# Performance work log

Hardware: AMD Instinct MI355X
Metric: run time of the kernel (lower is better)

## Reference

```python
import jax, jax.numpy as jnp
import numpy as np

EMB_DIM = 64
TREE_DIM = 128
VOCAB = 10000
SORT_VOCAB = 64
DEPTH = 8  # levels 0..8; leaves are level 0, root is level DEPTH
N_TREES = 256


def _tree_topology(depth):
    # perfect binary tree, nodes laid out leaves-first so the root is the LAST node
    level_sizes = [2 ** (depth - l) for l in range(depth + 1)]
    offsets = np.cumsum([0] + level_sizes)
    n = int(offsets[-1])  # 2^(depth+1)-1
    node_order = np.concatenate([np.full(level_sizes[l], l, np.int64) for l in range(depth + 1)])
    par, chi, eo = [], [], []
    for l in range(1, depth + 1):
        p = offsets[l] + np.arange(level_sizes[l])
        c0 = offsets[l - 1] + 2 * np.arange(level_sizes[l])
        par.append(np.repeat(p, 2))
        chi.append(np.stack([c0, c0 + 1], 1).reshape(-1))
        eo.append(np.full(2 * level_sizes[l], l, np.int64))
    return n, node_order, np.concatenate(par), np.concatenate(chi), np.concatenate(eo)


def setup_inputs():
    key = jax.random.key(0)
    ks = jax.random.split(key, 16)
    n, no, par, chi, eo = _tree_topology(DEPTH)
    offs = np.arange(N_TREES, dtype=np.int64) * n
    node_order = jnp.asarray(np.tile(no, N_TREES))
    parent_idx = jnp.asarray((par[None, :] + offs[:, None]).reshape(-1))
    child_idx = jnp.asarray((chi[None, :] + offs[:, None]).reshape(-1))
    edge_order = jnp.asarray(np.tile(eo, N_TREES))
    NT = N_TREES * n
    in_dim = 3 * EMB_DIM  # token_emb | sort_emb | const_emb

    def nrm(k, shape, s=0.05):
        return jax.random.normal(k, shape, jnp.float32) * s

    return dict(
        tokens_a=jax.random.randint(ks[0], (NT,), 0, VOCAB * 2),
        sorts_a=jax.random.randint(ks[1], (NT,), 0, SORT_VOCAB * 2),
        const_a=nrm(ks[2], (NT, EMB_DIM), 1.0),
        tokens_b=jax.random.randint(ks[3], (NT,), 0, VOCAB * 2),
        sorts_b=jax.random.randint(ks[4], (NT,), 0, SORT_VOCAB * 2),
        const_b=nrm(ks[5], (NT, EMB_DIM), 1.0),
        node_order=node_order, parent_idx=parent_idx, child_idx=child_idx,
        edge_order=edge_order, n_levels=DEPTH + 1, n_trees=N_TREES,
        emb=nrm(ks[6], (VOCAB * 2, EMB_DIM), 1.0),
        sort_emb_tab=nrm(ks[7], (SORT_VOCAB * 2, EMB_DIM), 1.0),
        W_iou=nrm(ks[8], (in_dim, 3 * TREE_DIM)),
        b_iou=jnp.zeros((3 * TREE_DIM,), jnp.float32),
        U_iou=nrm(ks[9], (TREE_DIM, 3 * TREE_DIM)),
        W_f=nrm(ks[10], (in_dim, TREE_DIM)),
        b_f=jnp.zeros((TREE_DIM,), jnp.float32),
        U_f=nrm(ks[11], (TREE_DIM, TREE_DIM)),
        fc1_w=nrm(ks[12], (2 * TREE_DIM + 1, TREE_DIM)),
        fc1_b=jnp.zeros((TREE_DIM,), jnp.float32),
        fc2_w=nrm(ks[13], (TREE_DIM, 2)),
        fc2_b=jnp.zeros((2,), jnp.float32),
    )


def _treelstm(feat, node_order, parent_idx, child_idx, edge_order, n_levels,
              W_iou, b_iou, U_iou, W_f, b_f, U_f):
    # child-sum TreeLSTM, level-synchronous from leaves (level 0) to root.
    N = feat.shape[0]
    td = U_f.shape[0]
    h = jnp.zeros((N, td), feat.dtype)
    c = jnp.zeros((N, td), feat.dtype)
    wiou_x = feat @ W_iou + b_iou  # [N, 3*td], hoisted out of the level loop
    wf_x = feat @ W_f + b_f        # [N, td]
    for t in range(n_levels):
        nmask = (node_order == t)[:, None]
        emask = (edge_order == t)[:, None].astype(feat.dtype)
        ch = h[child_idx]  # [E, td]
        cc = c[child_idx]
        h_sum = jax.ops.segment_sum(ch * emask, parent_idx, num_segments=N)
        f = jax.nn.sigmoid(wf_x[parent_idx] + ch @ U_f)  # per-edge forget gate
        c_sum = jax.ops.segment_sum(f * cc * emask, parent_idx, num_segments=N)
        i, o, u = jnp.split(wiou_x + h_sum @ U_iou, 3, axis=1)
        c_new = jax.nn.sigmoid(i) * jnp.tanh(u) + c_sum
        h_new = jax.nn.sigmoid(o) * jnp.tanh(c_new)
        h = jnp.where(nmask, h_new, h)
        c = jnp.where(nmask, c_new, c)
    return h, c


def reference(tokens_a, sorts_a, const_a, tokens_b, sorts_b, const_b,
              node_order, parent_idx, child_idx, edge_order, n_levels, n_trees,
              emb, sort_emb_tab, W_iou, b_iou, U_iou, W_f, b_f, U_f,
              fc1_w, fc1_b, fc2_w, fc2_b):
    def tree_root_h(tokens, sorts, const):
        feat = jnp.concatenate([emb[tokens], sort_emb_tab[sorts], const], axis=1)
        h, _ = _treelstm(feat, node_order, parent_idx, child_idx, edge_order,
                         n_levels, W_iou, b_iou, U_iou, W_f, b_f, U_f)
        n_per = h.shape[0] // n_trees
        roots = jnp.arange(n_trees) * n_per + (n_per - 1)  # stack_last_h: root is last node
        return h[roots]
    ha = tree_root_h(tokens_a, sorts_a, const_a)  # [B, td]
    hb = tree_root_h(tokens_b, sorts_b, const_b)
    dotp = jnp.sum(ha * hb, axis=-1, keepdims=True)  # diag(ha @ hb.T)
    hcat = jnp.concatenate([ha, hb, dotp], axis=-1)  # [B, 2*td+1]
    logits = jax.nn.relu(hcat @ fc1_w + fc1_b) @ fc2_w + fc2_b  # [B, 2]
    return logits
```

## Files before the change

kernel.cpp:

```cpp
#include <hip/hip_runtime.h>
#include <stdint.h>
#include <stddef.h>

typedef unsigned short u16;
typedef unsigned long long u64;
typedef short bf16x8 __attribute__((ext_vector_type(8)));
typedef float f32x4 __attribute__((ext_vector_type(4)));

#define NTREES 256
#define NPT 511
#define TD 128
#define PLANE_E ((size_t)65536 * TD)

#define S_TOKA 0
#define S_SRTA 1
#define S_CSTA 2
#define S_TOKB 3
#define S_SRTB 4
#define S_CSTB 5
#define S_EMB  6
#define S_SORT 7
#define S_WIOU 8
#define S_BIOU 9
#define S_UIOU 10
// ... 103 lines not shown
  wf[tid] = v;
}

__global__ __launch_bounds__(256) void prep_w(const u64* __restrict__ tab,
    const int* __restrict__ flags, u16* __restrict__ wzhi, u16* __restrict__ wzlo,
    float* __restrict__ bz)
{
  const int fl = flags[0];
  const int tid = blockIdx.x * 256 + threadIdx.x;
  if (tid < 640) {
    bz[tid] = (tid < 384) ? ldin((const void*)tab[S_BIOU], tid, fl)
                          : ldin((const void*)tab[S_BF], (tid - 384) & 127, fl);
  }
  if (tid >= 640 * 448) return;
  const int n = tid / 448, k = tid - n * 448;
  float v;
  if (k < 192) {
    v = (n < 384) ? ldin((const void*)tab[S_WIOU], (size_t)k * 384 + n, fl)
                  : ldin((const void*)tab[S_WF],   (size_t)k * 128 + ((n - 384) & 127), fl);
  } else if (k < 320) {
    const int kk = k - 192;
    v = (n < 384) ? ldin((const void*)tab[S_UIOU], (size_t)kk * 384 + n, fl)
      : (n < 512) ? ldin((const void*)tab[S_UF],   (size_t)kk * 128 + (n - 384), fl) : 0.f;
  } else {
    const int kk = k - 320;
    v = (n < 384) ? ldin((const void*)tab[S_UIOU], (size_t)kk * 384 + n, fl)
      : (n < 512) ? 0.f : ldin((const void*)tab[S_UF], (size_t)kk * 128 + (n - 512), fl);
  }
  const u16 hi = f2bf(v);
  wzhi[(size_t)n * 448 + k] = hi;
  wzlo[(size_t)n * 448 + k] = f2bf(v - bf2f(hi));
}

template<bool LEAF>
__global__ __launch_bounds__(512) void gemm_level_k(
    const u64* __restrict__ tab, const int* __restrict__ flags,
    const u16* __restrict__ wzhi, const u16* __restrict__ wzlo,
    const float* __restrict__ bz,
    u16* __restrict__ hhi, u16* __restrict__ hlo, float* __restrict__ cc,
    const int T, const int soArg, const int slotPerSide)
{
  constexpr int NKS = LEAF ? 6 : 14;
  constexpr int NG  = LEAF ? 3 : 5;
  __shared__ __align__(16) u16 Ah[2][4][64][8];
  __shared__ __align__(16) u16 Al[2][4][64][8];

  const int so = soArg + 3 * blockIdx.y;
  const size_t sb = (size_t)slotPerSide * blockIdx.y * TD;
  u16* hps = hhi + sb;
  u16* lps = hlo + sb;
  float* cps = cc + sb;
  const void* tokens = (const void*)tab[so + 0];
  const void* sorts  = (const void*)tab[so + 1];
  const void* cstp   = (const void*)tab[so + 2];
  const void* emb    = (const void*)tab[S_EMB];
  const void* sortt  = (const void*)tab[S_SORT];
  const int fl = flags[0], ti = flags[1], si = flags[2];
  const int tid = threadIdx.x, l = tid & 63, w = tid >> 6, lr = l & 15, lq = l >> 4;
  const int m0 = blockIdx.x * 64;
  const int lpt = 8 - T, mask = (1 << lpt) - 1, offp = 512 - (1 << (9 - T));

  const int srow = tid & 63, skq = tid >> 6;
  const int sm = m0 + srow;
  const int stree = sm >> lpt, sj = sm & mask;
  const size_t snode = (size_t)stree * NPT + offp + sj;
  int tok = ldint(tokens, snode, ti); tok = tok < 0 ? 0 : (tok > 19999 ? 19999 : tok);
  int srt = ldint(sorts,  snode, si); srt = srt < 0 ? 0 : (srt > 127 ? 127 : srt);
  size_t sc0 = 0, sc1 = 0;
  if (!LEAF) { sc0 = ((size_t)sm) << T; sc1 = sc0 + ((size_t)1 << (T - 1)); }

  auto stage = [&](int ks, int buf) {
    const int kg = ks * 32 + skq * 4;
    u16 hi4[4], lo4[4];
    if (LEAF || kg < 192) {
      if (fl) {
        const float* src;
        if (kg < 64)       src = (const float*)emb   + (size_t)tok * 64 + kg;
        else if (kg < 128) src = (const float*)sortt + (size_t)srt * 64 + (kg - 64);
        else               src = (const float*)cstp  + snode * 64 + (kg - 128);
        const float4 v = *(const float4*)src;
        const float xv[4] = {v.x, v.y, v.z, v.w};
#pragma unroll
        for (int j = 0; j < 4; ++j) {
          hi4[j] = f2bf(xv[j]);
          lo4[j] = f2bf(xv[j] - bf2f(hi4[j]));
        }
      } else {
        const u16* src;
        if (kg < 64)       src = (const u16*)emb   + (size_t)tok * 64 + kg;
        else if (kg < 128) src = (const u16*)sortt + (size_t)srt * 64 + (kg - 64);
        else               src = (const u16*)cstp  + snode * 64 + (kg - 128);
#pragma unroll
        for (int j = 0; j < 4; ++j) { hi4[j] = src[j]; lo4[j] = 0; }
      }
    } else {
      const size_t cslot = (kg < 320) ? sc0 : sc1;
      const int off = (kg < 320) ? (kg - 192) : (kg - 320);
      *(uint2*)hi4 = *(const uint2*)(hps + cslot * TD + off);
      *(uint2*)lo4 = *(const uint2*)(lps + cslot * TD + off);
    }
    *(uint2*)&Ah[buf][skq >> 1][srow][(skq & 1) * 4] = *(const uint2*)hi4;
    *(uint2*)&Al[buf][skq >> 1][srow][(skq & 1) * 4] = *(const uint2*)lo4;
  };

  f32x4 acc[4][NG];
#pragma unroll
  for (int mf = 0; mf < 4; ++mf)
#pragma unroll
    for (int g = 0; g < NG; ++g) acc[mf][g] = f32x4{0.f, 0.f, 0.f, 0.f};

  stage(0, 0);
  for (int ks = 0; ks < NKS; ++ks) {
    __syncthreads();
    if (ks + 1 < NKS) stage(ks + 1, (ks + 1) & 1);
    const int k0 = ks * 32;
    const int buf = ks & 1;
    bf16x8 ah[4], al[4];
#pragma unroll
    for (int mf = 0; mf < 4; ++mf) {
      ah[mf] = *(const bf16x8*)&Ah[buf][lq][mf * 16 + lr][0];
      al[mf] = *(const bf16x8*)&Al[buf][lq][mf * 16 + lr][0];
    }
#pragma unroll
    for (int g = 0; g < NG; ++g) {
      if (!LEAF) {
        if (g == 3 && k0 >= 320) continue;
        if (g == 4 && k0 >= 192 && k0 < 320) continue;
      }
      const size_t boff = (size_t)((g * 8 + w) * 16 + lr) * 448 + k0 + lq * 8;
      const bf16x8 bh = *(const bf16x8*)&wzhi[boff];
      const bf16x8 bl = *(const bf16x8*)&wzlo[boff];
#pragma unroll
      for (int mf = 0; mf < 4; ++mf) {
        acc[mf][g] = __builtin_amdgcn_mfma_f32_16x16x32_bf16(ah[mf], bh, acc[mf][g], 0, 0, 0);
        acc[mf][g] = __builtin_amdgcn_mfma_f32_16x16x32_bf16(al[mf], bh, acc[mf][g], 0, 0, 0);
        acc[mf][g] = __builtin_amdgcn_mfma_f32_16x16x32_bf16(ah[mf], bl, acc[mf][g], 0, 0, 0);
      }
    }
  }

  const int d = w * 16 + lr;
  const float bi = bz[d], bo = bz[128 + d], bu = bz[256 + d];
  float bf0 = 0.f, bf1 = 0.f;
  if (!LEAF) { bf0 = bz[384 + d]; bf1 = bz[512 + d]; }
#pragma unroll
  for (int mf = 0; mf < 4; ++mf) {
#pragma unroll
    for (int rr = 0; rr < 4; ++rr) {
      const int row = mf * 16 + lq * 4 + rr;
      const int m = m0 + row;
      const size_t ps = LEAF ? (size_t)m : (((size_t)m) << T);
      const float iv = acc[mf][0][rr] + bi;
      const float ov = acc[mf][1][rr] + bo;
      const float uv = acc[mf][2][rr] + bu;
      float cn = sigm(iv) * tanhf(uv);
      if (!LEAF) {
        const size_t c1s = ps + ((size_t)1 << (T - 1));
        cn += sigm(acc[mf][3][rr] + bf0) * cps[ps * TD + d]
            + sigm(acc[mf][4][rr] + bf1) * cps[c1s * TD + d];
      }
      cps[ps * TD + d] = cn;
      const float hv = sigm(ov) * tanhf(cn);
      const u16 hh = f2bf(hv);
      hps[ps * TD + d] = hh;
      lps[ps * TD + d] = f2bf(hv - bf2f(hh));
    }
  }
}

template<int L>
__global__ __launch_bounds__(128) void bottom_k(const u64* __restrict__ tab,
    const int* __restrict__ flags, const float* __restrict__ wf,
    float* __restrict__ h, float* __restrict__ c, const int so)
{
  constexpr int G = 16 >> L;
  __shared__ float sfeat[16][192];
  __shared__ float childh[16][128];
  const void* tokens = (const void*)tab[so + 0];
  const void* sorts  = (const void*)tab[so + 1];
  const void* cst    = (const void*)tab[so + 2];
  const void* emb    = (const void*)tab[S_EMB];
  const void* sortt  = (const void*)tab[S_SORT];
  const int d = threadIdx.x;
  const int fl = flags[0], ti = flags[1], si = flags[2];
  const int m0 = blockIdx.x * G;

  const float bi  = wf[O_BIOU + d];
  const float bo  = wf[O_BIOU + 128 + d];
  const float bu  = wf[O_BIOU + 256 + d];
  const float bf_ = wf[O_BF + d];

  for (int idx = d; idx < 16 * 192; idx += 128) {
    const int g = idx / 192, k = idx - g * 192;
    const int gl = (m0 << L) + g;
    const int tree = gl >> 8, j = gl & 255;
    const size_t node = (size_t)tree * NPT + j;
    float v;
    if (k < 64) {
      int tk = ldint(tokens, node, ti); tk = tk < 0 ? 0 : (tk > 19999 ? 19999 : tk);
// ... 255 lines not shown
    const u16* __restrict__ hhi, const u16* __restrict__ hlo,
    const float* __restrict__ wf, const u64 rb, float* __restrict__ out)
{
  __shared__ float sa[128], sb[128], red[2], r0s[2], r1s[2];
  const int t = blockIdx.x, d = threadIdx.x;
  const float av = ha[t * 128 + d];
  const size_t idx = rb + (((size_t)t) << 8) * TD + d;
  const float bv = bf2f(hhi[idx]) + bf2f(hlo[idx]);
  sa[d] = av; sb[d] = bv;
  float pdt = av * bv;
#pragma unroll
  for (int off = 32; off; off >>= 1) pdt += __shfl_down(pdt, off);
  if ((d & 63) == 0) red[d >> 6] = pdt;
  __syncthreads();
  const float dotp = red[0] + red[1];
  float r = wf[O_B1 + d];
  for (int k = 0; k < 128; ++k) r = fmaf(sa[k], wf[O_W1 + (size_t)k * 128 + d], r);
  for (int k = 0; k < 128; ++k) r = fmaf(sb[k], wf[O_W1 + (size_t)(128 + k) * 128 + d], r);
  r = fmaf(dotp, wf[O_W1 + (size_t)256 * 128 + d], r);
  r = fmaxf(r, 0.f);
  float o0 = r * wf[O_W2 + (size_t)d * 2];
  float o1 = r * wf[O_W2 + (size_t)d * 2 + 1];
#pragma unroll
  for (int off = 32; off; off >>= 1) { o0 += __shfl_down(o0, off); o1 += __shfl_down(o1, off); }
  if ((d & 63) == 0) { r0s[d >> 6] = o0; r1s[d >> 6] = o1; }
  __syncthreads();
  if (d == 0) {
    out[t * 2]     = r0s[0] + r0s[1] + wf[O_B2];
    out[t * 2 + 1] = r1s[0] + r1s[1] + wf[O_B2 + 1];
  }
}

static void run_gemm_levels(const u64* tab, const int* flags, const u16* wzhi,
                            const u16* wzlo, const float* bz,
                            u16* hhi, u16* hlo, float* cc,
                            int soArg, int slotPerSide, int nsides, hipStream_t stream)
{
  gemm_level_k<true><<<dim3(1024, nsides), 512, 0, stream>>>(
      tab, flags, wzhi, wzlo, bz, hhi, hlo, cc, 0, soArg, slotPerSide);
  for (int T = 1; T <= 8; ++T) {
    const int blocks = (NTREES << (8 - T)) / 64;
    gemm_level_k<false><<<dim3(blocks, nsides), 512, 0, stream>>>(
        tab, flags, wzhi, wzlo, bz, hhi, hlo, cc, T, soArg, slotPerSide);
  }
}

static void run_side_valu(int L, const u64* tab, const int* flags, const float* wf,
                          float* h, float* c, int so, hipStream_t stream)
{
  const int nb = (NTREES << (8 - L)) / (16 >> L);
  switch (L) {
    case 1: bottom_k<1><<<nb, 128, 0, stream>>>(tab, flags, wf, h, c, so); break;
    case 2: bottom_k<2><<<nb, 128, 0, stream>>>(tab, flags, wf, h, c, so); break;
    case 3: bottom_k<3><<<nb, 128, 0, stream>>>(tab, flags, wf, h, c, so); break;
    default: bottom_k<4><<<nb, 128, 0, stream>>>(tab, flags, wf, h, c, so); break;
  }
  for (int t = L + 1; t <= 8; ++t) {
    const int NL = NTREES << (8 - t);
    level_k<<<NL / 8, 128, 0, stream>>>(tab, flags, wf, h, c, so,
        8 - t, 512 - (1 << (9 - t)), t - L);
  }
}

extern "C" void kernel_launch(void* const* d_in, const int* in_sizes, int n_in,
                              void* d_out, int out_size, void* d_ws, size_t ws_size,
                              hipStream_t stream)
{
  ArgPack ap;
  ap.n = n_in < 32 ? n_in : 32;
  for (int i = 0; i < 32; ++i) {
    ap.p[i]  = (i < n_in) ? (u64)d_in[i] : 0ull;
    ap.sz[i] = (i < n_in) ? in_sizes[i] : 0;
  }

  char* p = (char*)d_ws;
  auto take = [&](size_t bytes){ char* q = p; p += (bytes + 255) & ~(size_t)255; return q; };

  u64*   tab   = (u64*)take(18 * 8);
  int*   flags = (int*)take(256);
  float* wfb   = (float*)take((size_t)W_TOTAL * 4);
  u16*   wzhi  = (u16*)take((size_t)640 * 448 * 2);
  u16*   wzlo  = (u16*)take((size_t)640 * 448 * 2);
  float* bz    = (float*)take(640 * 4);
  float* ha    = (float*)take((size_t)NTREES * TD * 4);
  const size_t fixedB = (size_t)(p - (char*)d_ws);

  const size_t sideB = PLANE_E * (2 + 2 + 4);
  const size_t need_conc = fixedB + 2 * sideB + (1 << 16);
  const size_t need_seq  = fixedB + 1 * sideB + (1 << 16);

  resolve_k<<<1, 64, 0, stream>>>(ap, tab, flags);
  prep_k<<<(W_TOTAL + 255) / 256, 256, 0, stream>>>(tab, flags, wfb);

  if (ws_size >= need_seq) {
    prep_w<<<(640 * 448 + 255) / 256, 256, 0, stream>>>(tab, flags, wzhi, wzlo, bz);
    const int nsides = (ws_size >= need_conc) ? 2 : 1;
    u16*   hhi = (u16*)take((size_t)nsides * PLANE_E * 2);
    u16*   hlo = (u16*)take((size_t)nsides * PLANE_E * 2);
    float* cc  = (float*)take((size_t)nsides * PLANE_E * 4);
    if (nsides == 2) {
      run_gemm_levels(tab, flags, wzhi, wzlo, bz, hhi, hlo, cc, S_TOKA, 65536, 2, stream);
      roots_split<<<(NTREES * TD) / 256, 256, 0, stream>>>(hhi, hlo, ha);
      final_split<<<NTREES, 128, 0, stream>>>(ha, hhi, hlo, wfb, (u64)PLANE_E, (float*)d_out);
    } else {
      run_gemm_levels(tab, flags, wzhi, wzlo, bz, hhi, hlo, cc, S_TOKA, 0, 1, stream);
      roots_split<<<(NTREES * TD) / 256, 256, 0, stream>>>(hhi, hlo, ha);
      run_gemm_levels(tab, flags, wzhi, wzlo, bz, hhi, hlo, cc, S_TOKB, 0, 1, stream);
      final_split<<<NTREES, 128, 0, stream>>>(ha, hhi, hlo, wfb, 0ull, (float*)d_out);
    }
    return;
  }

  int L = 1;
  while (L < 4) {
    const size_t need = fixedB + 2 * (((size_t)(NTREES << (8 - L))) * TD * 4 + 256) + 1024;
    if (ws_size >= need) break;
    ++L;
  }
  const int SH = 8 - L;
  const size_t hcB = ((size_t)(NTREES << SH)) * TD * 4;
  float* h = (float*)take(hcB);
  float* c = (float*)take(hcB);
  run_side_valu(L, tab, flags, wfb, h, c, S_TOKA, stream);
  roots_k<<<(NTREES * TD) / 256, 256, 0, stream>>>(h, ha, SH);
  run_side_valu(L, tab, flags, wfb, h, c, S_TOKB, stream);
  final_k<<<NTREES, 128, 0, stream>>>(ha, h, wfb, 0L, SH, (float*)d_out);
}
```

Before: 878.1 us.

## Fuse upper tree levels into one per-tree kernel and widen GEMM k-staging

Levels 3 through 8 are merged into a single tail kernel with one block per tree. Each block loops over the levels, with block-level syncs standing in for kernel boundaries, which removes six launches and the small, underfilled grids at the top of the tree. The level GEMM kernel now stages 64-wide k slices with 16-byte loads and fully unrolls the k loop, halving the barrier count. It also reorders the hi/lo MFMA sequence. The tail kernel runs only 256 blocks per side with 32-row tiles, many of them masked at high levels, so its occupancy is low.

```diff
diff --git a/kernel.cpp b/kernel.cpp
--- a/kernel.cpp
+++ b/kernel.cpp
@@ -167,10 +167,10 @@
     u16* __restrict__ hhi, u16* __restrict__ hlo, float* __restrict__ cc,
     const int T, const int soArg, const int slotPerSide)
 {
-  constexpr int NKS = LEAF ? 6 : 14;
-  constexpr int NG  = LEAF ? 3 : 5;
-  __shared__ __align__(16) u16 Ah[2][4][64][8];
-  __shared__ __align__(16) u16 Al[2][4][64][8];
+  constexpr int NI = LEAF ? 3 : 7;
+  constexpr int NG = LEAF ? 3 : 5;
+  __shared__ __align__(16) u16 Ah[2][2][4][64][8];
+  __shared__ __align__(16) u16 Al[2][2][4][64][8];
 
   const int so = soArg + 3 * blockIdx.y;
   const size_t sb = (size_t)slotPerSide * blockIdx.y * TD;
@@ -187,7 +187,8 @@
   const int m0 = blockIdx.x * 64;
   const int lpt = 8 - T, mask = (1 << lpt) - 1, offp = 512 - (1 << (9 - T));
 
-  const int srow = tid & 63, skq = tid >> 6;
+  const int srow = tid & 63, skoct = tid >> 6;
+  const int skh = skoct >> 2, slq = skoct & 3;
   const int sm = m0 + srow;
   const int stree = sm >> lpt, sj = sm & mask;
   const size_t snode = (size_t)stree * NPT + offp + sj;
@@ -196,38 +197,40 @@
   size_t sc0 = 0, sc1 = 0;
   if (!LEAF) { sc0 = ((size_t)sm) << T; sc1 = sc0 + ((size_t)1 << (T - 1)); }
 
-  auto stage = [&](int ks, int buf) {
-    const int kg = ks * 32 + skq * 4;
-    u16 hi4[4], lo4[4];
+  auto stage = [&](int iv2, int buf) {
+    const int kg = iv2 * 64 + skoct * 8;
+    u16 hi8[8], lo8[8];
     if (LEAF || kg < 192) {
       if (fl) {
         const float* src;
         if (kg < 64)       src = (const float*)emb   + (size_t)tok * 64 + kg;
         else if (kg < 128) src = (const float*)sortt + (size_t)srt * 64 + (kg - 64);
         else               src = (const float*)cstp  + snode * 64 + (kg - 128);
-        const float4 v = *(const float4*)src;
-        const float xv[4] = {v.x, v.y, v.z, v.w};
-#pragma unroll
-        for (int j = 0; j < 4; ++j) {
-          hi4[j] = f2bf(xv[j]);
-          lo4[j] = f2bf(xv[j] - bf2f(hi4[j]));
+        const float4 v0 = *(const float4*)src;
+        const float4 v1 = *(const float4*)(src + 4);
+        const float xv[8] = {v0.x, v0.y, v0.z, v0.w, v1.x, v1.y, v1.z, v1.w};
+#pragma unroll
+        for (int j = 0; j < 8; ++j) {
+          hi8[j] = f2bf(xv[j]);
+          lo8[j] = f2bf(xv[j] - bf2f(hi8[j]));
         }
       } else {
         const u16* src;
         if (kg < 64)       src = (const u16*)emb   + (size_t)tok * 64 + kg;
         else if (kg < 128) src = (const u16*)sortt + (size_t)srt * 64 + (kg - 64);
         else               src = (const u16*)cstp  + snode * 64 + (kg - 128);
-#pragma unroll
-        for (int j = 0; j < 4; ++j) { hi4[j] = src[j]; lo4[j] = 0; }
+        *(uint4*)hi8 = *(const uint4*)src;
+#pragma unroll
+        for (int j = 0; j < 8; ++j) lo8[j] = 0;
       }
     } else {
-      const size_t cslot = (kg < 320) ? sc0 : sc1;
+      const size_t cs = (kg < 320) ? sc0 : sc1;
       const int off = (kg < 320) ? (kg - 192) : (kg - 320);
-      *(uint2*)hi4 = *(const uint2*)(hps + cslot * TD + off);
-      *(uint2*)lo4 = *(const uint2*)(lps + cslot * TD + off);
-    }
-    *(uint2*)&Ah[buf][skq >> 1][srow][(skq & 1) * 4] = *(const uint2*)hi4;
-    *(uint2*)&Al[buf][skq >> 1][srow][(skq & 1) * 4] = *(const uint2*)lo4;
+      *(uint4*)hi8 = *(const uint4*)(hps + cs * TD + off);
+      *(uint4*)lo8 = *(const uint4*)(lps + cs * TD + off);
+    }
+    *(uint4*)&Ah[buf][skh][slq][srow][0] = *(const uint4*)hi8;
+    *(uint4*)&Al[buf][skh][slq][srow][0] = *(const uint4*)lo8;
   };
 
   f32x4 acc[4][NG];
@@ -237,31 +240,46 @@
     for (int g = 0; g < NG; ++g) acc[mf][g] = f32x4{0.f, 0.f, 0.f, 0.f};
 
   stage(0, 0);
-  for (int ks = 0; ks < NKS; ++ks) {
+#pragma unroll
+  for (int iv2 = 0; iv2 < NI; ++iv2) {
     __syncthreads();
-    if (ks + 1 < NKS) stage(ks + 1, (ks + 1) & 1);
-    const int k0 = ks * 32;
-    const int buf = ks & 1;
-    bf16x8 ah[4], al[4];
-#pragma unroll
-    for (int mf = 0; mf < 4; ++mf) {
-      ah[mf] = *(const bf16x8*)&Ah[buf][lq][mf * 16 + lr][0];
-      al[mf] = *(const bf16x8*)&Al[buf][lq][mf * 16 + lr][0];
-    }
-#pragma unroll
-    for (int g = 0; g < NG; ++g) {
-      if (!LEAF) {
-        if (g == 3 && k0 >= 320) continue;
-        if (g == 4 && k0 >= 192 && k0 < 320) continue;
-      }
-      const size_t boff = (size_t)((g * 8 + w) * 16 + lr) * 448 + k0 + lq * 8;
-      const bf16x8 bh = *(const bf16x8*)&wzhi[boff];
-      const bf16x8 bl = *(const bf16x8*)&wzlo[boff];
+    if (iv2 + 1 < NI) stage(iv2 + 1, (iv2 + 1) & 1);
+    const int buf = iv2 & 1;
+#pragma unroll
+    for (int kh = 0; kh < 2; ++kh) {
+      const int k0 = iv2 * 64 + kh * 32;
+      bf16x8 ah[4], al[4];
 #pragma unroll
       for (int mf = 0; mf < 4; ++mf) {
-        acc[mf][g] = __builtin_amdgcn_mfma_f32_16x16x32_bf16(ah[mf], bh, acc[mf][g], 0, 0, 0);
-        acc[mf][g] = __builtin_amdgcn_mfma_f32_16x16x32_bf16(al[mf], bh, acc[mf][g], 0, 0, 0);
-        acc[mf][g] = __builtin_amdgcn_mfma_f32_16x16x32_bf16(ah[mf], bl, acc[mf][g], 0, 0, 0);
+        ah[mf] = *(const bf16x8*)&Ah[buf][kh][lq][mf * 16 + lr][0];
+        al[mf] = *(const bf16x8*)&Al[buf][kh][lq][mf * 16 + lr][0];
+      }
+#pragma unroll
+      for (int g = 0; g < NG; ++g) {
+        if (!LEAF) {
+          if (g == 3 && k0 >= 320) continue;
+          if (g == 4 && k0 >= 192 && k0 < 320) continue;
+        }
+        const size_t boff = (size_t)((g * 8 + w) * 16 + lr) * 448 + k0 + lq * 8;
+        const bf16x8 bh = *(const bf16x8*)&wzhi[boff];
+#pragma unroll
+        for (int mf = 0; mf < 4; ++mf)
+          acc[mf][g] = __builtin_amdgcn_mfma_f32_16x16x32_bf16(ah[mf], bh, acc[mf][g], 0, 0, 0);
+#pragma unroll
+        for (int mf = 0; mf < 4; ++mf)
+          acc[mf][g] = __builtin_amdgcn_mfma_f32_16x16x32_bf16(al[mf], bh, acc[mf][g], 0, 0, 0);
+      }
+#pragma unroll
+      for (int g = 0; g < NG; ++g) {
+        if (!LEAF) {
+          if (g == 3 && k0 >= 320) continue;
+          if (g == 4 && k0 >= 192 && k0 < 320) continue;
+        }
+        const size_t boff = (size_t)((g * 8 + w) * 16 + lr) * 448 + k0 + lq * 8;
+        const bf16x8 blv = *(const bf16x8*)&wzlo[boff];
+#pragma unroll
+        for (int mf = 0; mf < 4; ++mf)
+          acc[mf][g] = __builtin_amdgcn_mfma_f32_16x16x32_bf16(ah[mf], blv, acc[mf][g], 0, 0, 0);
       }
     }
   }
@@ -277,21 +295,167 @@
       const int row = mf * 16 + lq * 4 + rr;
       const int m = m0 + row;
       const size_t ps = LEAF ? (size_t)m : (((size_t)m) << T);
-      const float iv = acc[mf][0][rr] + bi;
-      const float ov = acc[mf][1][rr] + bo;
-      const float uv = acc[mf][2][rr] + bu;
-      float cn = sigm(iv) * tanhf(uv);
+      const float va = acc[mf][0][rr] + bi;
+      const float vo = acc[mf][1][rr] + bo;
+      const float vu = acc[mf][2][rr] + bu;
+      float cn = sigm(va) * tanhf(vu);
       if (!LEAF) {
         const size_t c1s = ps + ((size_t)1 << (T - 1));
         cn += sigm(acc[mf][3][rr] + bf0) * cps[ps * TD + d]
             + sigm(acc[mf][4][rr] + bf1) * cps[c1s * TD + d];
       }
       cps[ps * TD + d] = cn;
-      const float hv = sigm(ov) * tanhf(cn);
+      const float hv = sigm(vo) * tanhf(cn);
       const u16 hh = f2bf(hv);
       hps[ps * TD + d] = hh;
       lps[ps * TD + d] = f2bf(hv - bf2f(hh));
     }
+  }
+}
+
+__global__ __launch_bounds__(256) void tail_k(
+    const u64* __restrict__ tab, const int* __restrict__ flags,
+    const u16* __restrict__ wzhi, const u16* __restrict__ wzlo,
+    const float* __restrict__ bz,
+    u16* __restrict__ hhi, u16* __restrict__ hlo, float* __restrict__ cc,
+    const int soArg, const int slotPerSide)
+{
+  __shared__ __align__(16) u16 Ah[2][2][4][32][8];
+  __shared__ __align__(16) u16 Al[2][2][4][32][8];
+
+  const int so = soArg + 3 * blockIdx.y;
+  const size_t sb = (size_t)slotPerSide * blockIdx.y * TD;
+  u16* hps = hhi + sb;
+  u16* lps = hlo + sb;
+  float* cps = cc + sb;
+  const void* tokens = (const void*)tab[so + 0];
+  const void* sorts  = (const void*)tab[so + 1];
+  const void* cstp   = (const void*)tab[so + 2];
+  const void* emb    = (const void*)tab[S_EMB];
+  const void* sortt  = (const void*)tab[S_SORT];
+  const int fl = flags[0], ti = flags[1], si = flags[2];
+  const int tid = threadIdx.x, l = tid & 63, w = tid >> 6, lr = l & 15, lq = l >> 4;
+  const int tree = blockIdx.x;
+  const int srow = tid & 31, skoct = tid >> 5;
+  const int skh = skoct >> 2, slq = skoct & 3;
+
+  for (int T = 3; T <= 8; ++T) {
+    const int nn = 256 >> T;
+    const int offp = 512 - (1 << (9 - T));
+    const int jc = srow < nn ? srow : nn - 1;
+    const size_t snode = (size_t)tree * NPT + offp + jc;
+    int tok = ldint(tokens, snode, ti); tok = tok < 0 ? 0 : (tok > 19999 ? 19999 : tok);
+    int srt = ldint(sorts,  snode, si); srt = srt < 0 ? 0 : (srt > 127 ? 127 : srt);
+    const int ms = (tree << (8 - T)) + jc;
+    const size_t sc0 = ((size_t)ms) << T;
+    const size_t sc1 = sc0 + ((size_t)1 << (T - 1));
+
+    auto stage = [&](int iv2, int buf) {
+      const int kg = iv2 * 64 + skoct * 8;
+      u16 hi8[8], lo8[8];
+      if (kg < 192) {
+        if (fl) {
+          const float* src;
+          if (kg < 64)       src = (const float*)emb   + (size_t)tok * 64 + kg;
+          else if (kg < 128) src = (const float*)sortt + (size_t)srt * 64 + (kg - 64);
+          else               src = (const float*)cstp  + snode * 64 + (kg - 128);
+          const float4 v0 = *(const float4*)src;
+          const float4 v1 = *(const float4*)(src + 4);
+          const float xv[8] = {v0.x, v0.y, v0.z, v0.w, v1.x, v1.y, v1.z, v1.w};
+#pragma unroll
+          for (int jj = 0; jj < 8; ++jj) {
+            hi8[jj] = f2bf(xv[jj]);
+            lo8[jj] = f2bf(xv[jj] - bf2f(hi8[jj]));
+          }
+        } else {
+          const u16* src;
+          if (kg < 64)       src = (const u16*)emb   + (size_t)tok * 64 + kg;
+          else if (kg < 128) src = (const u16*)sortt + (size_t)srt * 64 + (kg - 64);
+          else               src = (const u16*)cstp  + snode * 64 + (kg - 128);
+          *(uint4*)hi8 = *(const uint4*)src;
+#pragma unroll
+          for (int jj = 0; jj < 8; ++jj) lo8[jj] = 0;
+        }
+      } else {
+        const size_t cs = (kg < 320) ? sc0 : sc1;
+        const int off = (kg < 320) ? (kg - 192) : (kg - 320);
+        *(uint4*)hi8 = *(const uint4*)(hps + cs * TD + off);
+        *(uint4*)lo8 = *(const uint4*)(lps + cs * TD + off);
+      }
+      *(uint4*)&Ah[buf][skh][slq][srow][0] = *(const uint4*)hi8;
+      *(uint4*)&Al[buf][skh][slq][srow][0] = *(const uint4*)lo8;
+    };
+
+    f32x4 acc[2][10];
+#pragma unroll
+    for (int mf = 0; mf < 2; ++mf)
+#pragma unroll
+      for (int j2 = 0; j2 < 10; ++j2) acc[mf][j2] = f32x4{0.f, 0.f, 0.f, 0.f};
+
+    stage(0, 0);
+#pragma unroll
+    for (int iv2 = 0; iv2 < 7; ++iv2) {
+      __syncthreads();
+      if (iv2 < 6) stage(iv2 + 1, (iv2 + 1) & 1);
+      const int buf = iv2 & 1;
+#pragma unroll
+      for (int kh = 0; kh < 2; ++kh) {
+        const int k0 = iv2 * 64 + kh * 32;
+        bf16x8 ah[2], al[2];
+#pragma unroll
+        for (int mf = 0; mf < 2; ++mf) {
+          ah[mf] = *(const bf16x8*)&Ah[buf][kh][lq][mf * 16 + lr][0];
+          al[mf] = *(const bf16x8*)&Al[buf][kh][lq][mf * 16 + lr][0];
+        }
+#pragma unroll
+        for (int j2 = 0; j2 < 10; ++j2) {
+          const int f = w + 4 * j2;
+          const int g = f >> 3;
+          if (g == 3 && k0 >= 320) continue;
+          if (g == 4 && k0 >= 192 && k0 < 320) continue;
+          const size_t boff = (size_t)(f * 16 + lr) * 448 + k0 + lq * 8;
+          const bf16x8 bh  = *(const bf16x8*)&wzhi[boff];
+          const bf16x8 blv = *(const bf16x8*)&wzlo[boff];
+          acc[0][j2] = __builtin_amdgcn_mfma_f32_16x16x32_bf16(ah[0], bh,  acc[0][j2], 0, 0, 0);
+          acc[1][j2] = __builtin_amdgcn_mfma_f32_16x16x32_bf16(ah[1], bh,  acc[1][j2], 0, 0, 0);
+          acc[0][j2] = __builtin_amdgcn_mfma_f32_16x16x32_bf16(al[0], bh,  acc[0][j2], 0, 0, 0);
+          acc[1][j2] = __builtin_amdgcn_mfma_f32_16x16x32_bf16(al[1], bh,  acc[1][j2], 0, 0, 0);
+          acc[0][j2] = __builtin_amdgcn_mfma_f32_16x16x32_bf16(ah[0], blv, acc[0][j2], 0, 0, 0);
+          acc[1][j2] = __builtin_amdgcn_mfma_f32_16x16x32_bf16(ah[1], blv, acc[1][j2], 0, 0, 0);
+        }
+      }
+    }
+
+#pragma unroll
+    for (int cidx = 0; cidx < 2; ++cidx) {
+      const int d = (w + cidx * 4) * 16 + lr;
+      const float bi = bz[d], bo = bz[128 + d], bu = bz[256 + d];
+      const float bf0 = bz[384 + d], bf1 = bz[512 + d];
+#pragma unroll
+      for (int mf = 0; mf < 2; ++mf) {
+#pragma unroll
+        for (int rr = 0; rr < 4; ++rr) {
+          const int row = mf * 16 + lq * 4 + rr;
+          if (row < nn) {
+            const int m = (tree << (8 - T)) + row;
+            const size_t ps = ((size_t)m) << T;
+            const size_t c1s = ps + ((size_t)1 << (T - 1));
+            const float va = acc[mf][0 + cidx][rr] + bi;
+            const float vo = acc[mf][2 + cidx][rr] + bo;
+            const float vu = acc[mf][4 + cidx][rr] + bu;
+            float cn = sigm(va) * tanhf(vu)
+                     + sigm(acc[mf][6 + cidx][rr] + bf0) * cps[ps * TD + d]
+                     + sigm(acc[mf][8 + cidx][rr] + bf1) * cps[c1s * TD + d];
+            cps[ps * TD + d] = cn;
+            const float hv = sigm(vo) * tanhf(cn);
+            const u16 hh = f2bf(hv);
+            hps[ps * TD + d] = hh;
+            lps[ps * TD + d] = f2bf(hv - bf2f(hh));
+          }
+        }
+      }
+    }
+    __syncthreads();
   }
 }
 
@@ -619,11 +783,12 @@
 {
   gemm_level_k<true><<<dim3(1024, nsides), 512, 0, stream>>>(
       tab, flags, wzhi, wzlo, bz, hhi, hlo, cc, 0, soArg, slotPerSide);
-  for (int T = 1; T <= 8; ++T) {
-    const int blocks = (NTREES << (8 - T)) / 64;
-    gemm_level_k<false><<<dim3(blocks, nsides), 512, 0, stream>>>(
-        tab, flags, wzhi, wzlo, bz, hhi, hlo, cc, T, soArg, slotPerSide);
-  }
+  gemm_level_k<false><<<dim3(512, nsides), 512, 0, stream>>>(
+      tab, flags, wzhi, wzlo, bz, hhi, hlo, cc, 1, soArg, slotPerSide);
+  gemm_level_k<false><<<dim3(256, nsides), 512, 0, stream>>>(
+      tab, flags, wzhi, wzlo, bz, hhi, hlo, cc, 2, soArg, slotPerSide);
+  tail_k<<<dim3(256, nsides), 256, 0, stream>>>(
+      tab, flags, wzhi, wzlo, bz, hhi, hlo, cc, soArg, slotPerSide);
 }
 
 static void run_side_valu(int L, const u64* tab, const int* flags, const float* wf,
```

New measurement: 1.347 ms. +53.4%, slower.

## Use small-batch FP32 VALU kernel for upper tree levels instead of MFMA GEMM

Applied to the files above, without the earlier changes.

The per-level MFMA GEMM kernel is kept for leaves and the first two internal levels. Levels 3 through 8 now use a new level_tail_k kernel, where each 128-thread block handles 8 nodes with FP32 FMAs against the FP32 weights. The upper levels have few nodes, so 64-row GEMM tiles launched very few blocks; 8-node blocks spread that work over more CUs. The trade is re-reading full weight matrices per block through VALU instead of using split-bf16 MFMA, and the arithmetic now differs slightly between the two paths.

```diff
diff --git a/kernel.cpp b/kernel.cpp
--- a/kernel.cpp
+++ b/kernel.cpp
@@ -277,21 +277,120 @@
       const int row = mf * 16 + lq * 4 + rr;
       const int m = m0 + row;
       const size_t ps = LEAF ? (size_t)m : (((size_t)m) << T);
-      const float iv = acc[mf][0][rr] + bi;
-      const float ov = acc[mf][1][rr] + bo;
-      const float uv = acc[mf][2][rr] + bu;
-      float cn = sigm(iv) * tanhf(uv);
+      const float va = acc[mf][0][rr] + bi;
+      const float vo = acc[mf][1][rr] + bo;
+      const float vu = acc[mf][2][rr] + bu;
+      float cn = sigm(va) * tanhf(vu);
       if (!LEAF) {
         const size_t c1s = ps + ((size_t)1 << (T - 1));
         cn += sigm(acc[mf][3][rr] + bf0) * cps[ps * TD + d]
             + sigm(acc[mf][4][rr] + bf1) * cps[c1s * TD + d];
       }
       cps[ps * TD + d] = cn;
-      const float hv = sigm(ov) * tanhf(cn);
+      const float hv = sigm(vo) * tanhf(cn);
       const u16 hh = f2bf(hv);
       hps[ps * TD + d] = hh;
       lps[ps * TD + d] = f2bf(hv - bf2f(hh));
     }
+  }
+}
+
+__global__ __launch_bounds__(128) void level_tail_k(const u64* __restrict__ tab,
+    const int* __restrict__ flags, const float* __restrict__ wf,
+    u16* __restrict__ hhi, u16* __restrict__ hlo, float* __restrict__ cc,
+    const int soArg, const int slotPerSide, const int T)
+{
+  __shared__ float sf[8][192];
+  __shared__ float sh0[8][128], sh1[8][128];
+  const int so = soArg + 3 * blockIdx.y;
+  const size_t sb = (size_t)slotPerSide * blockIdx.y * TD;
+  u16* hps = hhi + sb;
+  u16* lps = hlo + sb;
+  float* cps = cc + sb;
+  const void* tokens = (const void*)tab[so + 0];
+  const void* sorts  = (const void*)tab[so + 1];
+  const void* cst    = (const void*)tab[so + 2];
+  const void* emb    = (const void*)tab[S_EMB];
+  const void* sortt  = (const void*)tab[S_SORT];
+  const int d = threadIdx.x;
+  const int fl = flags[0], ti = flags[1], si = flags[2];
+  const int m0 = blockIdx.x * 8;
+  const int lpt = 8 - T, mask = (1 << lpt) - 1, offp = 512 - (1 << (9 - T));
+
+  for (int idx = d; idx < 8 * 192; idx += 128) {
+    const int g = idx / 192, k = idx - g * 192;
+    const int m = m0 + g;
+    const int tree = m >> lpt, j = m & mask;
+    const size_t node = (size_t)tree * NPT + offp + j;
+    float v;
+    if (k < 64) {
+      int tk = ldint(tokens, node, ti); tk = tk < 0 ? 0 : (tk > 19999 ? 19999 : tk);
+      v = ldin(emb, (size_t)tk * 64 + k, fl);
+    } else if (k < 128) {
+      int sr = ldint(sorts, node, si); sr = sr < 0 ? 0 : (sr > 127 ? 127 : sr);
+      v = ldin(sortt, (size_t)sr * 64 + (k - 64), fl);
+    } else v = ldin(cst, node * 64 + (k - 128), fl);
+    sf[g][k] = v;
+  }
+  for (int idx = d; idx < 8 * 128; idx += 128) {
+    const int g = idx >> 7, k = idx & 127;
+    const size_t s0 = ((size_t)(m0 + g)) << T;
+    const size_t s1 = s0 + ((size_t)1 << (T - 1));
+    sh0[g][k] = bf2f(hps[s0 * TD + k]) + bf2f(lps[s0 * TD + k]);
+    sh1[g][k] = bf2f(hps[s1 * TD + k]) + bf2f(lps[s1 * TD + k]);
+  }
+  __syncthreads();
+
+  const float bi  = wf[O_BIOU + d];
+  const float bo  = wf[O_BIOU + 128 + d];
+  const float bu  = wf[O_BIOU + 256 + d];
+  const float bf_ = wf[O_BF + d];
+
+  float ai[8], ao[8], au[8], af[8], f0[8], f1[8];
+#pragma unroll
+  for (int g = 0; g < 8; ++g) { ai[g] = bi; ao[g] = bo; au[g] = bu; af[g] = bf_; f0[g] = 0.f; f1[g] = 0.f; }
+
+  for (int k = 0; k < 192; ++k) {
+    const float wi = wf[O_WIOU + (size_t)k * 384 + d];
+    const float wo = wf[O_WIOU + (size_t)k * 384 + 128 + d];
+    const float wu = wf[O_WIOU + (size_t)k * 384 + 256 + d];
+    const float wfc = wf[O_WF + (size_t)k * 128 + d];
+#pragma unroll
+    for (int g = 0; g < 8; ++g) {
+      const float x = sf[g][k];
+      ai[g] = fmaf(x, wi, ai[g]);
+      ao[g] = fmaf(x, wo, ao[g]);
+      au[g] = fmaf(x, wu, au[g]);
+      af[g] = fmaf(x, wfc, af[g]);
+    }
+  }
+  for (int k = 0; k < 128; ++k) {
+    const float ui = wf[O_UIOU + (size_t)k * 384 + d];
+    const float uo = wf[O_UIOU + (size_t)k * 384 + 128 + d];
+    const float uu = wf[O_UIOU + (size_t)k * 384 + 256 + d];
+    const float uf = wf[O_UF + (size_t)k * 128 + d];
+#pragma unroll
+    for (int g = 0; g < 8; ++g) {
+      const float s0 = sh0[g][k], s1 = sh1[g][k], s = s0 + s1;
+      ai[g] = fmaf(s,  ui, ai[g]);
+      ao[g] = fmaf(s,  uo, ao[g]);
+      au[g] = fmaf(s,  uu, au[g]);
+      f0[g] = fmaf(s0, uf, f0[g]);
+      f1[g] = fmaf(s1, uf, f1[g]);
+    }
+  }
+#pragma unroll
+  for (int g = 0; g < 8; ++g) {
+    const size_t ps = ((size_t)(m0 + g)) << T;
+    const size_t s1 = ps + ((size_t)1 << (T - 1));
+    float cn = sigm(ai[g]) * tanhf(au[g])
+             + sigm(af[g] + f0[g]) * cps[ps * TD + d]
+             + sigm(af[g] + f1[g]) * cps[s1 * TD + d];
+    cps[ps * TD + d] = cn;
+    const float hv = sigm(ao[g]) * tanhf(cn);
+    const u16 hh = f2bf(hv);
+    hps[ps * TD + d] = hh;
+    lps[ps * TD + d] = f2bf(hv - bf2f(hh));
   }
 }
 
@@ -613,16 +712,20 @@
 }
 
 static void run_gemm_levels(const u64* tab, const int* flags, const u16* wzhi,
-                            const u16* wzlo, const float* bz,
+                            const u16* wzlo, const float* bz, const float* wfb,
                             u16* hhi, u16* hlo, float* cc,
                             int soArg, int slotPerSide, int nsides, hipStream_t stream)
 {
   gemm_level_k<true><<<dim3(1024, nsides), 512, 0, stream>>>(
       tab, flags, wzhi, wzlo, bz, hhi, hlo, cc, 0, soArg, slotPerSide);
-  for (int T = 1; T <= 8; ++T) {
-    const int blocks = (NTREES << (8 - T)) / 64;
-    gemm_level_k<false><<<dim3(blocks, nsides), 512, 0, stream>>>(
-        tab, flags, wzhi, wzlo, bz, hhi, hlo, cc, T, soArg, slotPerSide);
+  gemm_level_k<false><<<dim3(512, nsides), 512, 0, stream>>>(
+      tab, flags, wzhi, wzlo, bz, hhi, hlo, cc, 1, soArg, slotPerSide);
+  gemm_level_k<false><<<dim3(256, nsides), 512, 0, stream>>>(
+      tab, flags, wzhi, wzlo, bz, hhi, hlo, cc, 2, soArg, slotPerSide);
+  for (int T = 3; T <= 8; ++T) {
+    const int blocks = (NTREES << (8 - T)) / 8;
+    level_tail_k<<<dim3(blocks, nsides), 128, 0, stream>>>(
+        tab, flags, wfb, hhi, hlo, cc, soArg, slotPerSide, T);
   }
 }
 
@@ -680,13 +783,13 @@
     u16*   hlo = (u16*)take((size_t)nsides * PLANE_E * 2);
     float* cc  = (float*)take((size_t)nsides * PLANE_E * 4);
     if (nsides == 2) {
-      run_gemm_levels(tab, flags, wzhi, wzlo, bz, hhi, hlo, cc, S_TOKA, 65536, 2, stream);
+      run_gemm_levels(tab, flags, wzhi, wzlo, bz, wfb, hhi, hlo, cc, S_TOKA, 65536, 2, stream);
       roots_split<<<(NTREES * TD) / 256, 256, 0, stream>>>(hhi, hlo, ha);
       final_split<<<NTREES, 128, 0, stream>>>(ha, hhi, hlo, wfb, (u64)PLANE_E, (float*)d_out);
     } else {
-      run_gemm_levels(tab, flags, wzhi, wzlo, bz, hhi, hlo, cc, S_TOKA, 0, 1, stream);
+      run_gemm_levels(tab, flags, wzhi, wzlo, bz, wfb, hhi, hlo, cc, S_TOKA, 0, 1, stream);
       roots_split<<<(NTREES * TD) / 256, 256, 0, stream>>>(hhi, hlo, ha);
-      run_gemm_levels(tab, flags, wzhi, wzlo, bz, hhi, hlo, cc, S_TOKB, 0, 1, stream);
+      run_gemm_levels(tab, flags, wzhi, wzlo, bz, wfb, hhi, hlo, cc, S_TOKB, 0, 1, stream);
       final_split<<<NTREES, 128, 0, stream>>>(ha, hhi, hlo, wfb, 0ull, (float*)d_out);
     }
     return;
```

After: 1.025 ms. 1.17x slower.

## Fuse leaf and first two internal tree levels into one kernel via LDS

Applied to the files above, without the earlier changes.

Adds a kernel that computes the leaf level and levels 1 and 2 of the TreeLSTM for a 64-leaf subtree per block. Child h and c stay in shared memory between levels instead of going through global memory, and two kernel launches per side are dropped. The cost is that the upper levels use only half and then a quarter of the threads for staging and fewer MFMA rows, so occupancy falls with the larger LDS footprint.

```diff
diff --git a/kernel.cpp b/kernel.cpp
--- a/kernel.cpp
+++ b/kernel.cpp
@@ -159,6 +159,294 @@
   wzlo[(size_t)n * 448 + k] = f2bf(v - bf2f(hi));
 }
 
+__global__ __launch_bounds__(512) void fused_bottom_k(
+    const u64* __restrict__ tab, const int* __restrict__ flags,
+    const u16* __restrict__ wzhi, const u16* __restrict__ wzlo,
+    const float* __restrict__ bz,
+    u16* __restrict__ hhi, u16* __restrict__ hlo, float* __restrict__ cc,
+    const int soArg, const int slotPerSide)
+{
+  __shared__ __align__(16) u16 Ah[2][4][64][8];
+  __shared__ __align__(16) u16 Al[2][4][64][8];
+  __shared__ __align__(16) u16 HB[64][128];
+  __shared__ __align__(16) u16 LB[64][128];
+  __shared__ float CB[64][128];
+
+  const int so = soArg + 3 * blockIdx.y;
+  const size_t sb = (size_t)slotPerSide * blockIdx.y * TD;
+  u16* hps = hhi + sb;
+  u16* lps = hlo + sb;
+  float* cps = cc + sb;
+  const void* tokens = (const void*)tab[so + 0];
+  const void* sorts  = (const void*)tab[so + 1];
+  const void* cstp   = (const void*)tab[so + 2];
+  const void* emb    = (const void*)tab[S_EMB];
+  const void* sortt  = (const void*)tab[S_SORT];
+  const int fl = flags[0], ti = flags[1], si = flags[2];
+  const int tid = threadIdx.x, l = tid & 63, w = tid >> 6, lr = l & 15, lq = l >> 4;
+  const int blk = blockIdx.x;
+  const int d = w * 16 + lr;
+  const float bi = bz[d], bo = bz[128 + d], bu = bz[256 + d];
+  const float bf0 = bz[384 + d], bf1 = bz[512 + d];
+
+  {
+    const int srow = tid & 63, skq = tid >> 6;
+    const int gl = blk * 64 + srow;
+    const int tree = gl >> 8, jj = gl & 255;
+    const size_t node = (size_t)tree * NPT + jj;
+    int tok = ldint(tokens, node, ti); tok = tok < 0 ? 0 : (tok > 19999 ? 19999 : tok);
+    int srt = ldint(sorts,  node, si); srt = srt < 0 ? 0 : (srt > 127 ? 127 : srt);
+
+    auto stage0 = [&](int ks, int buf) {
+      const int kg = ks * 32 + skq * 4;
+      u16 hi4[4], lo4[4];
+      if (fl) {
+        const float* src;
+        if (kg < 64)       src = (const float*)emb   + (size_t)tok * 64 + kg;
+        else if (kg < 128) src = (const float*)sortt + (size_t)srt * 64 + (kg - 64);
+        else               src = (const float*)cstp  + node * 64 + (kg - 128);
+        const float4 v = *(const float4*)src;
+        const float xv[4] = {v.x, v.y, v.z, v.w};
+#pragma unroll
+        for (int q = 0; q < 4; ++q) {
+          hi4[q] = f2bf(xv[q]);
+          lo4[q] = f2bf(xv[q] - bf2f(hi4[q]));
+        }
+      } else {
+        const u16* src;
+        if (kg < 64)       src = (const u16*)emb   + (size_t)tok * 64 + kg;
+        else if (kg < 128) src = (const u16*)sortt + (size_t)srt * 64 + (kg - 64);
+        else               src = (const u16*)cstp  + node * 64 + (kg - 128);
+#pragma unroll
+        for (int q = 0; q < 4; ++q) { hi4[q] = src[q]; lo4[q] = 0; }
+      }
+      *(uint2*)&Ah[buf][skq >> 1][srow][(skq & 1) * 4] = *(const uint2*)hi4;
+      *(uint2*)&Al[buf][skq >> 1][srow][(skq & 1) * 4] = *(const uint2*)lo4;
+    };
+
+    f32x4 acc[4][3];
+#pragma unroll
+    for (int mf = 0; mf < 4; ++mf)
+#pragma unroll
+      for (int g = 0; g < 3; ++g) acc[mf][g] = f32x4{0.f,0.f,0.f,0.f};
+
+    stage0(0, 0);
+    for (int ks = 0; ks < 6; ++ks) {
+      __syncthreads();
+      if (ks + 1 < 6) stage0(ks + 1, (ks + 1) & 1);
+      const int k0 = ks * 32, buf = ks & 1;
+      bf16x8 ah[4], al[4];
+#pragma unroll
+      for (int mf = 0; mf < 4; ++mf) {
+        ah[mf] = *(const bf16x8*)&Ah[buf][lq][mf * 16 + lr][0];
+        al[mf] = *(const bf16x8*)&Al[buf][lq][mf * 16 + lr][0];
+      }
+#pragma unroll
+      for (int g = 0; g < 3; ++g) {
+        const size_t boff = (size_t)((g * 8 + w) * 16 + lr) * 448 + k0 + lq * 8;
+        const bf16x8 bh = *(const bf16x8*)&wzhi[boff];
+        const bf16x8 bl = *(const bf16x8*)&wzlo[boff];
+#pragma unroll
+        for (int mf = 0; mf < 4; ++mf) {
+          acc[mf][g] = __builtin_amdgcn_mfma_f32_16x16x32_bf16(ah[mf], bh, acc[mf][g], 0, 0, 0);
+          acc[mf][g] = __builtin_amdgcn_mfma_f32_16x16x32_bf16(al[mf], bh, acc[mf][g], 0, 0, 0);
+          acc[mf][g] = __builtin_amdgcn_mfma_f32_16x16x32_bf16(ah[mf], bl, acc[mf][g], 0, 0, 0);
+        }
+      }
+    }
+#pragma unroll
+    for (int mf = 0; mf < 4; ++mf) {
+#pragma unroll
+      for (int rr = 0; rr < 4; ++rr) {
+        const int row = mf * 16 + lq * 4 + rr;
+        const float cn = sigm(acc[mf][0][rr] + bi) * tanhf(acc[mf][2][rr] + bu);
+        const float hv = sigm(acc[mf][1][rr] + bo) * tanhf(cn);
+        const u16 hh = f2bf(hv);
+        HB[row][d] = hh;
+        LB[row][d] = f2bf(hv - bf2f(hh));
+        CB[row][d] = cn;
+      }
+    }
+  }
+  __syncthreads();
+
+  {
+    const int srow = tid & 31, skq = (tid >> 5) & 7;
+    const int m1 = blk * 32 + srow;
+    const int tree = m1 >> 7, jj = m1 & 127;
+    const size_t node = (size_t)tree * NPT + 256 + jj;
+    int tok = ldint(tokens, node, ti); tok = tok < 0 ? 0 : (tok > 19999 ? 19999 : tok);
+    int srt = ldint(sorts,  node, si); srt = srt < 0 ? 0 : (srt > 127 ? 127 : srt);
+
+    auto stage1 = [&](int ks, int buf) {
+      if (tid >= 256) return;
+      const int kg = ks * 32 + skq * 4;
+      u16 hi4[4], lo4[4];
+      if (kg < 192) {
+        if (fl) {
+          const float* src;
+          if (kg < 64)       src = (const float*)emb   + (size_t)tok * 64 + kg;
+          else if (kg < 128) src = (const float*)sortt + (size_t)srt * 64 + (kg - 64);
+          else               src = (const float*)cstp  + node * 64 + (kg - 128);
+          const float4 v = *(const float4*)src;
+          const float xv[4] = {v.x, v.y, v.z, v.w};
+#pragma unroll
+          for (int q = 0; q < 4; ++q) {
+            hi4[q] = f2bf(xv[q]);
+            lo4[q] = f2bf(xv[q] - bf2f(hi4[q]));
+          }
+        } else {
+          const u16* src;
+          if (kg < 64)       src = (const u16*)emb   + (size_t)tok * 64 + kg;
+          else if (kg < 128) src = (const u16*)sortt + (size_t)srt * 64 + (kg - 64);
+          else               src = (const u16*)cstp  + node * 64 + (kg - 128);
+#pragma unroll
+          for (int q = 0; q < 4; ++q) { hi4[q] = src[q]; lo4[q] = 0; }
+        }
+      } else {
+        const int crow = 2 * srow + (kg >= 320 ? 1 : 0);
+        const int off = kg - (kg < 320 ? 192 : 320);
+        *(uint2*)hi4 = *(const uint2*)&HB[crow][off];
+        *(uint2*)lo4 = *(const uint2*)&LB[crow][off];
+      }
+      *(uint2*)&Ah[buf][skq >> 1][srow][(skq & 1) * 4] = *(const uint2*)hi4;
+      *(uint2*)&Al[buf][skq >> 1][srow][(skq & 1) * 4] = *(const uint2*)lo4;
+    };
+
+    f32x4 acc[2][5];
+#pragma unroll
+    for (int mf = 0; mf < 2; ++mf)
+#pragma unroll
+      for (int g = 0; g < 5; ++g) acc[mf][g] = f32x4{0.f,0.f,0.f,0.f};
+
+    stage1(0, 0);
+    for (int ks = 0; ks < 14; ++ks) {
+      __syncthreads();
+      if (ks + 1 < 14) stage1(ks + 1, (ks + 1) & 1);
+      const int k0 = ks * 32, buf = ks & 1;
+      bf16x8 ah[2], al[2];
+#pragma unroll
+      for (int mf = 0; mf < 2; ++mf) {
+        ah[mf] = *(const bf16x8*)&Ah[buf][lq][mf * 16 + lr][0];
+        al[mf] = *(const bf16x8*)&Al[buf][lq][mf * 16 + lr][0];
+      }
+#pragma unroll
+      for (int g = 0; g < 5; ++g) {
+        if (g == 3 && k0 >= 320) continue;
+        if (g == 4 && k0 >= 192 && k0 < 320) continue;
+        const size_t boff = (size_t)((g * 8 + w) * 16 + lr) * 448 + k0 + lq * 8;
+        const bf16x8 bh = *(const bf16x8*)&wzhi[boff];
+        const bf16x8 bl = *(const bf16x8*)&wzlo[boff];
+#pragma unroll
+        for (int mf = 0; mf < 2; ++mf) {
+          acc[mf][g] = __builtin_amdgcn_mfma_f32_16x16x32_bf16(ah[mf], bh, acc[mf][g], 0, 0, 0);
+          acc[mf][g] = __builtin_amdgcn_mfma_f32_16x16x32_bf16(al[mf], bh, acc[mf][g], 0, 0, 0);
+          acc[mf][g] = __builtin_amdgcn_mfma_f32_16x16x32_bf16(ah[mf], bl, acc[mf][g], 0, 0, 0);
+        }
+      }
+    }
+#pragma unroll
+    for (int mf = 0; mf < 2; ++mf) {
+#pragma unroll
+      for (int rr = 0; rr < 4; ++rr) {
+        const int row = mf * 16 + lq * 4 + rr;
+        const float f0 = sigm(acc[mf][3][rr] + bf0);
+        const float f1 = sigm(acc[mf][4][rr] + bf1);
+        const float cn = sigm(acc[mf][0][rr] + bi) * tanhf(acc[mf][2][rr] + bu)
+                       + f0 * CB[2 * row][d] + f1 * CB[2 * row + 1][d];
+        const float hv = sigm(acc[mf][1][rr] + bo) * tanhf(cn);
+        CB[2 * row][d] = cn;
+        const u16 hh = f2bf(hv);
+        HB[2 * row][d] = hh;
+        LB[2 * row][d] = f2bf(hv - bf2f(hh));
+      }
+    }
+  }
+  __syncthreads();
+
+  {
+    const int srow = tid & 15, skq = (tid >> 4) & 7;
+    const int m2 = blk * 16 + srow;
+    const int tree = m2 >> 6, jj = m2 & 63;
+    const size_t node = (size_t)tree * NPT + 384 + jj;
+    int tok = ldint(tokens, node, ti); tok = tok < 0 ? 0 : (tok > 19999 ? 19999 : tok);
+    int srt = ldint(sorts,  node, si); srt = srt < 0 ? 0 : (srt > 127 ? 127 : srt);
+
+    auto stage2 = [&](int ks, int buf) {
+      if (tid >= 128) return;
+      const int kg = ks * 32 + skq * 4;
+      u16 hi4[4], lo4[4];
+      if (kg < 192) {
+        if (fl) {
+          const float* src;
+          if (kg < 64)       src = (const float*)emb   + (size_t)tok * 64 + kg;
+          else if (kg < 128) src = (const float*)sortt + (size_t)srt * 64 + (kg - 64);
+          else               src = (const float*)cstp  + node * 64 + (kg - 128);
+          const float4 v = *(const float4*)src;
+          const float xv[4] = {v.x, v.y, v.z, v.w};
+#pragma unroll
+          for (int q = 0; q < 4; ++q) {
+            hi4[q] = f2bf(xv[q]);
+            lo4[q] = f2bf(xv[q] - bf2f(hi4[q]));
+          }
+        } else {
+          const u16* src;
+          if (kg < 64)       src = (const u16*)emb   + (size_t)tok * 64 + kg;
+          else if (kg < 128) src = (const u16*)sortt + (size_t)srt * 64 + (kg - 64);
+          else               src = (const u16*)cstp  + node * 64 + (kg - 128);
+#pragma unroll
+          for (int q = 0; q < 4; ++q) { hi4[q] = src[q]; lo4[q] = 0; }
+        }
+      } else {
+        const int crow = 4 * srow + (kg >= 320 ? 2 : 0);
+        const int off = kg - (kg < 320 ? 192 : 320);
+        *(uint2*)hi4 = *(const uint2*)&HB[crow][off];
+        *(uint2*)lo4 = *(const uint2*)&LB[crow][off];
+      }
+      *(uint2*)&Ah[buf][skq >> 1][srow][(skq & 1) * 4] = *(const uint2*)hi4;
+      *(uint2*)&Al[buf][skq >> 1][srow][(skq & 1) * 4] = *(const uint2*)lo4;
+    };
+
+    f32x4 acc[5];
+#pragma unroll
+    for (int g = 0; g < 5; ++g) acc[g] = f32x4{0.f,0.f,0.f,0.f};
+
+    stage2(0, 0);
+    for (int ks = 0; ks < 14; ++ks) {
+      __syncthreads();
+      if (ks + 1 < 14) stage2(ks + 1, (ks + 1) & 1);
+      const int k0 = ks * 32, buf = ks & 1;
+      const bf16x8 ah = *(const bf16x8*)&Ah[buf][lq][lr][0];
+      const bf16x8 al = *(const bf16x8*)&Al[buf][lq][lr][0];
+#pragma unroll
+      for (int g = 0; g < 5; ++g) {
+        if (g == 3 && k0 >= 320) continue;
+        if (g == 4 && k0 >= 192 && k0 < 320) continue;
+        const size_t boff = (size_t)((g * 8 + w) * 16 + lr) * 448 + k0 + lq * 8;
+        const bf16x8 bh = *(const bf16x8*)&wzhi[boff];
+        const bf16x8 bl = *(const bf16x8*)&wzlo[boff];
+        acc[g] = __builtin_amdgcn_mfma_f32_16x16x32_bf16(ah, bh, acc[g], 0, 0, 0);
+        acc[g] = __builtin_amdgcn_mfma_f32_16x16x32_bf16(al, bh, acc[g], 0, 0, 0);
+        acc[g] = __builtin_amdgcn_mfma_f32_16x16x32_bf16(ah, bl, acc[g], 0, 0, 0);
+      }
+    }
+#pragma unroll
+    for (int rr = 0; rr < 4; ++rr) {
+      const int row = lq * 4 + rr;
+      const float f0 = sigm(acc[3][rr] + bf0);
+      const float f1 = sigm(acc[4][rr] + bf1);
+      const float cn = sigm(acc[0][rr] + bi) * tanhf(acc[2][rr] + bu)
+                     + f0 * CB[4 * row][d] + f1 * CB[4 * row + 2][d];
+      const float hv = sigm(acc[1][rr] + bo) * tanhf(cn);
+      const size_t ps = ((size_t)(blk * 16 + row)) << 2;
+      cps[ps * TD + d] = cn;
+      const u16 hh = f2bf(hv);
+      hps[ps * TD + d] = hh;
+      lps[ps * TD + d] = f2bf(hv - bf2f(hh));
+    }
+  }
+}
+
 template<bool LEAF>
 __global__ __launch_bounds__(512) void gemm_level_k(
     const u64* __restrict__ tab, const int* __restrict__ flags,
@@ -277,17 +565,17 @@
       const int row = mf * 16 + lq * 4 + rr;
       const int m = m0 + row;
       const size_t ps = LEAF ? (size_t)m : (((size_t)m) << T);
-      const float iv = acc[mf][0][rr] + bi;
-      const float ov = acc[mf][1][rr] + bo;
-      const float uv = acc[mf][2][rr] + bu;
-      float cn = sigm(iv) * tanhf(uv);
+      const float va = acc[mf][0][rr] + bi;
+      const float vo = acc[mf][1][rr] + bo;
+      const float vu = acc[mf][2][rr] + bu;
+      float cn = sigm(va) * tanhf(vu);
       if (!LEAF) {
         const size_t c1s = ps + ((size_t)1 << (T - 1));
         cn += sigm(acc[mf][3][rr] + bf0) * cps[ps * TD + d]
             + sigm(acc[mf][4][rr] + bf1) * cps[c1s * TD + d];
       }
       cps[ps * TD + d] = cn;
-      const float hv = sigm(ov) * tanhf(cn);
+      const float hv = sigm(vo) * tanhf(cn);
       const u16 hh = f2bf(hv);
       hps[ps * TD + d] = hh;
       lps[ps * TD + d] = f2bf(hv - bf2f(hh));
@@ -617,9 +905,9 @@
                             u16* hhi, u16* hlo, float* cc,
                             int soArg, int slotPerSide, int nsides, hipStream_t stream)
 {
-  gemm_level_k<true><<<dim3(1024, nsides), 512, 0, stream>>>(
-      tab, flags, wzhi, wzlo, bz, hhi, hlo, cc, 0, soArg, slotPerSide);
-  for (int T = 1; T <= 8; ++T) {
+  fused_bottom_k<<<dim3(1024, nsides), 512, 0, stream>>>(
+      tab, flags, wzhi, wzlo, bz, hhi, hlo, cc, soArg, slotPerSide);
+  for (int T = 3; T <= 8; ++T) {
     const int blocks = (NTREES << (8 - T)) / 64;
     gemm_level_k<false><<<dim3(blocks, nsides), 512, 0, stream>>>(
         tab, flags, wzhi, wzlo, bz, hhi, hlo, cc, T, soArg, slotPerSide);
```

After: 1.115 ms. 1.27x slower.
